# Optimization experiments

Measured on AMD Instinct MI355X. Metric: run time of the kernel, lower is better.

Reference implementation:

```python
import jax, jax.numpy as jnp
import numpy as np

D = 1024      # d_model
H = 16        # n_heads
KVH = 4       # num_kv_heads
DH = D // H   # head_dim = 64
CHUNK = 256
SDIM = 128
MG = 8        # m_global
B, T = 4, 4096


def setup_inputs() -> dict:
    key = jax.random.key(0)
    ks = jax.random.split(key, 12)
    s = 0.02
    mk = lambda i, shape: jax.random.normal(ks[i], shape, jnp.float32) * s
    return dict(
        x=jax.random.normal(ks[0], (B, T, D), jnp.float32),
        state=jnp.zeros((B, SDIM), jnp.float32),
        Wq=mk(1, (D, D)), Wk=mk(2, (KVH * DH, D)), Wv=mk(3, (KVH * DH, D)),
        Wo=mk(4, (D, D)), bo=jnp.zeros((D,), jnp.float32),
        ln_attn_g=jnp.ones((D,), jnp.float32), ln_attn_b=jnp.zeros((D,), jnp.float32),
        ln_ffn_g=jnp.ones((D,), jnp.float32), ln_ffn_b=jnp.zeros((D,), jnp.float32),
        W1=mk(5, (4 * D, D)), b1=jnp.zeros((4 * D,), jnp.float32),
        W2=mk(6, (D, 4 * D)), b2=jnp.zeros((D,), jnp.float32),
        Wsp=mk(7, (SDIM, D)), bsp=jnp.zeros((SDIM,), jnp.float32),
        Wsi=mk(8, (D, SDIM)), bsi=jnp.zeros((D,), jnp.float32),
        gtok=mk(9, (MG, D)),
    )


def _ln(x, g, b):
    m = x.mean(-1, keepdims=True)
    v = ((x - m) ** 2).mean(-1, keepdims=True)
    return (x - m) / jnp.sqrt(v + 1e-5) * g + b


def reference(x, state, Wq, Wk, Wv, Wo, bo, ln_attn_g, ln_attn_b,
              ln_ffn_g, ln_ffn_b, W1, b1, W2, b2, Wsp, bsp, Wsi, bsi, gtok):
    Bn, Tn, Dn = x.shape
    nchunks = Tn // CHUNK
    Tc = MG + CHUNK            # tokens per attention call (globals + chunk)
    G = H // KVH               # query heads per KV head
    causal = jnp.tril(jnp.ones((Tc, Tc), bool))
    scale = 1.0 / np.sqrt(DH).astype(np.float32)

    def step(st, chunk):  # st:[B,SDIM], chunk:[B,CHUNK,D]
        h = _ln(chunk, ln_attn_g, ln_attn_b) + (st @ Wsi.T + bsi)[:, None, :]
        h_in = jnp.concatenate([jnp.broadcast_to(gtok, (Bn, MG, Dn)), h], axis=1)
        q = (h_in @ Wq.T).reshape(Bn, Tc, H, DH)
        k = (h_in @ Wk.T).reshape(Bn, Tc, KVH, DH)
        v = (h_in @ Wv.T).reshape(Bn, Tc, KVH, DH)
        # GQA: group query heads over shared KV heads
        qg = q.reshape(Bn, Tc, KVH, G, DH)
        scores = jnp.einsum('bqhgd,bkhd->bhgqk', qg * scale, k)
        scores = jnp.where(causal, scores, -jnp.inf)
        attn = jax.nn.softmax(scores, axis=-1)
        o = jnp.einsum('bhgqk,bkhd->bqhgd', attn, v).reshape(Bn, Tc, Dn)
        y = (o @ Wo.T + bo)[:, MG:, :]
        c = chunk + y
        ff = jax.nn.gelu(_ln(c, ln_ffn_g, ln_ffn_b) @ W1.T + b1, approximate=False) @ W2.T + b2
        c = c + ff
        new_st = c.mean(axis=1) @ Wsp.T + bsp
        return new_st, c

    chunks = x.reshape(Bn, nchunks, CHUNK, Dn).transpose(1, 0, 2, 3)
    final_state, outs = jax.lax.scan(step, state, chunks)
    y_full = outs.transpose(1, 0, 2, 3).reshape(Bn, Tn, Dn)
    return y_full, final_state
```

## Files before the change

### kernel.cpp

```cpp
#include <hip/hip_runtime.h>
#include <hip/hip_bf16.h>

#define Dm    1024
#define Hn    16
#define KVH   4
#define DH    64
#define CHUNK 256
#define SDIM  128
#define MG    8
#define Bn    4
#define Tn    4096
#define TC    264
#define NSTEP 16
#define TD    4194304L

typedef __attribute__((ext_vector_type(8))) short short8;
typedef __attribute__((ext_vector_type(4))) float floatx4;
typedef __hip_bfloat16 bf16;

__device__ __forceinline__ void gl16(const void* g, void* l) {
    using GP = const __attribute__((address_space(1))) char*;
    using LP = __attribute__((address_space(3))) char*;
    __builtin_amdgcn_global_load_lds((GP)g, (LP)l, 16, 0, 0);
}


__global__ __launch_bounds__(512) void vcopy_k(const float* __restrict__ s, float* __restrict__ d, int n) {
    int i = blockIdx.x * 512 + threadIdx.x;
    if (i < n) d[i] = s[i];
}

__global__ __launch_bounds__(256) void cvt_bf16_k(const float* __restrict__ s, bf16* __restrict__ d, int n4) {
    int i = blockIdx.x * 256 + threadIdx.x;
    if (i >= n4) return;
    float4 v = ((const float4*)s)[i];
    bf16* o = d + i * 4;
    o[0] = __float2bfloat16(v.x); o[1] = __float2bfloat16(v.y);
    o[2] = __float2bfloat16(v.z); o[3] = __float2bfloat16(v.w);
}

__global__ __launch_bounds__(256) void fill_globals_k(const float* __restrict__ gtok, bf16* __restrict__ h_in) {
    int idx = blockIdx.x * 256 + threadIdx.x;
    int b = idx >> 13, rd = idx & 8191;
    h_in[(long)b * (TC * Dm) + rd] = __float2bfloat16(gtok[rd]);
}

__global__ __launch_bounds__(64) void state_proj_k(const float* __restrict__ st, const float* __restrict__ Wsi,
                                                   const float* __restrict__ bsi, float* __restrict__ si) {
    int b = blockIdx.x, g = blockIdx.y;
    int d = g * 64 + threadIdx.x;
    const float* sr = st + b * SDIM;
    const float* wr = Wsi + (long)d * SDIM;
    float a = bsi[d];
#pragma unroll
    for (int k4 = 0; k4 < 32; ++k4) {
        float4 sv = *(const float4*)(sr + k4 * 4);
        float4 wv = *(const float4*)(wr + k4 * 4);
        a += sv.x * wv.x + sv.y * wv.y + sv.z * wv.z + sv.w * wv.w;
    }
    si[b * Dm + d] = a;
}

__global__ __launch_bounds__(256) void ln_rows_k(const float* __restrict__ in, long inS, long inRoff,
                                                 bf16* __restrict__ out, long outS, long outRoff,
                                                 const float* __restrict__ g, const float* __restrict__ be,
                                                 const float* __restrict__ add) {
    int r = blockIdx.x, b = blockIdx.y, tid = threadIdx.x;
    const float* row = in + (long)b * inS + (inRoff + r) * (long)Dm;
    float4 v = *(const float4*)(row + tid * 4);
    float s = v.x + v.y + v.z + v.w;
    float q = v.x * v.x + v.y * v.y + v.z * v.z + v.w * v.w;
    for (int off = 32; off > 0; off >>= 1) { s += __shfl_down(s, off); q += __shfl_down(q, off); }
    __shared__ float red[10];
    int w = tid >> 6;
    if ((tid & 63) == 0) { red[w] = s; red[4 + w] = q; }
    __syncthreads();
    if (tid == 0) {
        float ts = red[0] + red[1] + red[2] + red[3];
        float tq = red[4] + red[5] + red[6] + red[7];
        float mean = ts * (1.f / Dm);
        float var = tq * (1.f / Dm) - mean * mean;
        red[8] = mean;
        red[9] = rsqrtf(var + 1e-5f);
    }
    __syncthreads();
    float mean = red[8], rstd = red[9];
    int d = tid * 4;
    float4 gv = *(const float4*)(g + d);
    float4 bv = *(const float4*)(be + d);
    float o0 = (v.x - mean) * rstd * gv.x + bv.x;
    float o1 = (v.y - mean) * rstd * gv.y + bv.y;
    float o2 = (v.z - mean) * rstd * gv.z + bv.z;
    float o3 = (v.w - mean) * rstd * gv.w + bv.w;
    if (add) {
        float4 av = *(const float4*)(add + b * Dm + d);
        o0 += av.x; o1 += av.y; o2 += av.z; o3 += av.w;
    }
    bf16* orow = out + (long)b * outS + (outRoff + r) * (long)Dm + d;
    orow[0] = __float2bfloat16(o0); orow[1] = __float2bfloat16(o1);
    orow[2] = __float2bfloat16(o2); orow[3] = __float2bfloat16(o3);
}

template<int BN>
__global__ __launch_bounds__(256) void gemm64(
    const bf16* __restrict__ A, const bf16* __restrict__ W,
    int M, int N, int K, int kspan,
    bf16* __restrict__ Cb, int ldc, const float* __restrict__ bias, int gelu,
    float* __restrict__ Cpart, long partMN)
{
    constexpr int NSEG = 4 + BN / 16;
    constexpr int SEGW = NSEG / 4;
    constexpr int FC   = BN / 64;
    constexpr int WN   = BN / 4;
    __shared__ short S[2 * NSEG * 512];

    int tid = threadIdx.x;
    int w = tid >> 6, l = tid & 63;
    int m0 = blockIdx.y << 6, n0 = blockIdx.x * BN;
    int kb = blockIdx.z * kspan;

    const bf16* gp[SEGW];
    int so[SEGW];
#pragma unroll
    for (int si = 0; si < SEGW; ++si) {
        int s = w + si * 4;
        const bf16* base = (s < 4) ? (A + (long)(m0 + s * 16 + (l >> 2)) * K)
                                   : (W + (long)(n0 + (s - 4) * 16 + (l >> 2)) * K);
        gp[si] = base + ((l & 3) << 3) + kb;
        so[si] = s * 1024 + l * 16;
    }
    char* cS = (char*)S;
    constexpr int LDSB = NSEG * 1024;

    floatx4 acc[4][FC];
#pragma unroll
    for (int t = 0; t < 4; ++t)
#pragma unroll
        for (int u = 0; u < FC; ++u) acc[t][u] = (floatx4){0.f, 0.f, 0.f, 0.f};

    int arow = l & 15;
    int acol = (l >> 4) << 3;
    int nk = kspan >> 5;

#define STAGE(t)                                                     \
    {                                                                \
        int kt_ = (t) << 5;                                          \
        char* b_ = cS + (((t) & 1) ? LDSB : 0);                      \
        _Pragma("unroll")                                            \
        for (int si = 0; si < SEGW; ++si) gl16(gp[si] + kt_, b_ + so[si]); \
    }

    STAGE(0)
    for (int i = 0; i < nk; ++i) {
        if (i + 1 < nk) {
            STAGE(i + 1)
            if constexpr (SEGW == 2) asm volatile("s_waitcnt vmcnt(2)" ::: "memory");
            else                     asm volatile("s_waitcnt vmcnt(3)" ::: "memory");
        } else {
            asm volatile("s_waitcnt vmcnt(0)" ::: "memory");
        }
        __builtin_amdgcn_s_barrier();
        __builtin_amdgcn_sched_barrier(0);
        const short* buf = S + (i & 1) * (NSEG * 512);
        short8 a[4], b[FC];
#pragma unroll
        for (int t = 0; t < 4; ++t)
            a[t] = *(const short8*)&buf[(t * 16 + arow) * 32 + acol];
#pragma unroll
        for (int u = 0; u < FC; ++u)
            b[u] = *(const short8*)&buf[2048 + (w * WN + u * 16 + arow) * 32 + acol];
#pragma unroll
        for (int t = 0; t < 4; ++t)
#pragma unroll
            for (int u = 0; u < FC; ++u)
                acc[t][u] = __builtin_amdgcn_mfma_f32_16x16x32_bf16(a[t], b[u], acc[t][u], 0, 0, 0);
        __builtin_amdgcn_sched_barrier(0);
        __builtin_amdgcn_s_barrier();
    }
#undef STAGE

    int crow0 = m0 + ((l >> 4) << 2);
    int ccol0 = n0 + w * WN + (l & 15);
    if (Cpart) {
        float* pp = Cpart + (long)blockIdx.z * partMN;
#pragma unroll
        for (int t = 0; t < 4; ++t)
#pragma unroll
            for (int rr = 0; rr < 4; ++rr) {
                int m = crow0 + t * 16 + rr;
                if (m >= M) continue;
#pragma unroll
                for (int u = 0; u < FC; ++u)
                    pp[(long)m * N + ccol0 + u * 16] = acc[t][u][rr];
            }
    } else {
#pragma unroll
        for (int t = 0; t < 4; ++t)
#pragma unroll
            for (int rr = 0; rr < 4; ++rr) {
                int m = crow0 + t * 16 + rr;
                if (m >= M) continue;
                bf16* crow = Cb + (long)m * ldc;
#pragma unroll
                for (int u = 0; u < FC; ++u) {
                    int n = ccol0 + u * 16;
                    float v = acc[t][u][rr];
                    if (bias) v += bias[n];
                    if (gelu) v = 0.5f * v * (1.f + erff(v * 0.70710678118654752f));
                    crow[n] = __float2bfloat16(v);
                }
            }
    }
}

__global__ __launch_bounds__(256) void reduce_splitk_k(const float* __restrict__ part, int KS,
                                                       const float* __restrict__ bias,
                                                       const float* __restrict__ res,
                                                       float* __restrict__ out, long roff) {
    int e4 = blockIdx.x * 256 + threadIdx.x;
    int m = e4 >> 8, n4 = e4 & 255;
    float4 s = ((const float4*)part)[e4];
    for (int z = 1; z < KS; ++z) {
        float4 p = ((const float4*)(part + (long)z * 1048576))[e4];
        s.x += p.x; s.y += p.y; s.z += p.z; s.w += p.w;
    }
    float4 bv = ((const float4*)bias)[n4];
    long ro = (long)(m >> 8) * TD + (roff + (m & 255)) * 1024L + n4 * 4;
    float4 rv = *(const float4*)(res + ro);
    s.x += bv.x + rv.x; s.y += bv.y + rv.y; s.z += bv.z + rv.z; s.w += bv.w + rv.w;
    *(float4*)(out + ro) = s;
}

__global__ __launch_bounds__(256) void reduce_ln_k(const float* __restrict__ part,
                                                   const float* __restrict__ bo,
                                                   const float* __restrict__ x,
                                                   float* __restrict__ out, long roff,
                                                   const float* __restrict__ g,
                                                   const float* __restrict__ be,
                                                   bf16* __restrict__ t_ln) {
    int m = blockIdx.x;
    int b = m >> 8, r = m & 255;
    int tid = threadIdx.x;
    long ro = (long)b * TD + (roff + r) * 1024L + tid * 4;
    int pi = m * 256 + tid;
    float4 s  = ((const float4*)part)[pi];
    float4 p2 = ((const float4*)(part + 1048576))[pi];
    float4 bv = ((const float4*)bo)[tid];
    float4 rv = *(const float4*)(x + ro);
    float c0 = s.x + p2.x + bv.x + rv.x;
    float c1 = s.y + p2.y + bv.y + rv.y;
    float c2 = s.z + p2.z + bv.z + rv.z;
    float c3 = s.w + p2.w + bv.w + rv.w;
    *(float4*)(out + ro) = make_float4(c0, c1, c2, c3);
    float sum = c0 + c1 + c2 + c3;
    float sq  = c0 * c0 + c1 * c1 + c2 * c2 + c3 * c3;
    for (int off = 32; off > 0; off >>= 1) { sum += __shfl_down(sum, off); sq += __shfl_down(sq, off); }
    __shared__ float red[10];
    int w = tid >> 6;
    if ((tid & 63) == 0) { red[w] = sum; red[4 + w] = sq; }
    __syncthreads();
    if (tid == 0) {
        float ts = red[0] + red[1] + red[2] + red[3];
        float tq = red[4] + red[5] + red[6] + red[7];
        float mean = ts * (1.f / Dm);
        float var = tq * (1.f / Dm) - mean * mean;
        red[8] = mean;
        red[9] = rsqrtf(var + 1e-5f);
    }
    __syncthreads();
    float mean = red[8], rstd = red[9];
    float4 gv = ((const float4*)g)[tid];
    float4 bev = ((const float4*)be)[tid];
    bf16* orow = t_ln + (long)(b * CHUNK + r) * Dm + tid * 4;
    orow[0] = __float2bfloat16((c0 - mean) * rstd * gv.x + bev.x);
    orow[1] = __float2bfloat16((c1 - mean) * rstd * gv.y + bev.y);
    orow[2] = __float2bfloat16((c2 - mean) * rstd * gv.z + bev.z);
    orow[3] = __float2bfloat16((c3 - mean) * rstd * gv.w + bev.w);
}

__global__ __launch_bounds__(256) void attn_mfma_k(const bf16* __restrict__ qkv, bf16* __restrict__ o_mat) {
    int qc = blockIdx.x, head = blockIdx.y, b = blockIdx.z;
    int kvh = head >> 2;
    int tid = threadIdx.x, w = tid >> 6, l = tid & 63;
    int m16 = l & 15, h4 = l >> 4;

    __shared__ short Qs[64][64];
    __shared__ short Ks[64][64];
    __shared__ short Vt[64][64];
    __shared__ short Ps[4][16][64];

    const long rowq0 = (long)b * TC + MG + qc * 64;
    const bf16* kbase = qkv + ((long)b * TC) * 1536 + 1024 + kvh * DH;
    const bf16* vbase = kbase + 256;

#pragma unroll
    for (int p = 0; p < 2; ++p) {
        int rr = p * 32 + (tid >> 3);
        gl16(qkv + (rowq0 + rr) * 1536 + head * DH + (tid & 7) * 8, &Qs[rr][(tid & 7) * 8]);
    }

    float a_m[4] = {-1e30f, -1e30f, -1e30f, -1e30f};
    float a_l[4] = {0.f, 0.f, 0.f, 0.f};
    floatx4 acc_o[4];
#pragma unroll
    for (int dt = 0; dt < 4; ++dt) acc_o[dt] = (floatx4){0.f, 0.f, 0.f, 0.f};
    short8 aq[2];

    int qtok0 = MG + qc * 64 + w * 16 + h4 * 4;
    int ntiles = qc + 2;

    for (int t = 0; t < ntiles; ++t) {
        int jt = t * 64;
#pragma unroll
        for (int p = 0; p < 2; ++p) {
            int rr = p * 32 + (tid >> 3);
            int gk = min(jt + rr, TC - 1);
            gl16(kbase + (long)gk * 1536 + (tid & 7) * 8, &Ks[rr][(tid & 7) * 8]);
        }
#pragma unroll
        for (int p = 0; p < 2; ++p) {
            int cg = p * 4 + w;
            int gk = min(jt + l, TC - 1);
            short8 vv = *(const short8*)(vbase + (long)gk * 1536 + cg * 8);
#pragma unroll
            for (int e = 0; e < 8; ++e) Vt[cg * 8 + e][l] = vv[e];
        }
        __syncthreads();
        if (t == 0) {
            aq[0] = *(const short8*)&Qs[w * 16 + m16][h4 * 8];
            aq[1] = *(const short8*)&Qs[w * 16 + m16][32 + h4 * 8];
        }
        floatx4 s[4];
#pragma unroll
        for (int st = 0; st < 4; ++st) {
            s[st] = (floatx4){0.f, 0.f, 0.f, 0.f};
#pragma unroll
            for (int c = 0; c < 2; ++c) {
                short8 kf = *(const short8*)&Ks[st * 16 + m16][c * 32 + h4 * 8];
                s[st] = __builtin_amdgcn_mfma_f32_16x16x32_bf16(aq[c], kf, s[st], 0, 0, 0);
            }
        }
#pragma unroll
        for (int st = 0; st < 4; ++st) {
            int keyg = jt + st * 16 + m16;
#pragma unroll
            for (int r = 0; r < 4; ++r) {
                float v = s[st][r] * 0.125f;
                s[st][r] = (keyg > qtok0 + r) ? -1e30f : v;
            }
        }
#pragma unroll
        for (int r = 0; r < 4; ++r) {
            float tm = fmaxf(fmaxf(s[0][r], s[1][r]), fmaxf(s[2][r], s[3][r]));
            tm = fmaxf(tm, __shfl_xor(tm, 1));
            tm = fmaxf(tm, __shfl_xor(tm, 2));
            tm = fmaxf(tm, __shfl_xor(tm, 4));
            tm = fmaxf(tm, __shfl_xor(tm, 8));
            float mn = fmaxf(a_m[r], tm);
            float rs = __expf(a_m[r] - mn);
            a_m[r] = mn;
            float ps = 0.f;
#pragma unroll
            for (int st = 0; st < 4; ++st) {
                float p = __expf(s[st][r] - mn);
                s[st][r] = p;
                ps += p;
            }
            ps += __shfl_xor(ps, 1); ps += __shfl_xor(ps, 2);
            ps += __shfl_xor(ps, 4); ps += __shfl_xor(ps, 8);
            a_l[r] = a_l[r] * rs + ps;
#pragma unroll
            for (int dt = 0; dt < 4; ++dt) acc_o[dt][r] *= rs;
#pragma unroll
            for (int st = 0; st < 4; ++st) {
                bf16 hb = __float2bfloat16(s[st][r]);
                Ps[w][h4 * 4 + r][st * 16 + m16] = *reinterpret_cast<short*>(&hb);
            }
        }
#pragma unroll
        for (int c = 0; c < 2; ++c) {
            short8 ap = *(const short8*)&Ps[w][m16][c * 32 + h4 * 8];
#pragma unroll
            for (int dt = 0; dt < 4; ++dt) {
                short8 vf = *(const short8*)&Vt[dt * 16 + m16][c * 32 + h4 * 8];
                acc_o[dt] = __builtin_amdgcn_mfma_f32_16x16x32_bf16(ap, vf, acc_o[dt], 0, 0, 0);
            }
        }
        __syncthreads();
    }

#pragma unroll
    for (int r = 0; r < 4; ++r) {
        float inv = 1.f / a_l[r];
        long row = (long)b * CHUNK + qc * 64 + w * 16 + h4 * 4 + r;
#pragma unroll
        for (int dt = 0; dt < 4; ++dt)
            o_mat[row * Dm + head * DH + dt * 16 + m16] = __float2bfloat16(acc_o[dt][r] * inv);
    }
}

__global__ __launch_bounds__(256) void col_part_k(const float* __restrict__ c, long stepOff,
                                                  float* __restrict__ colp) {
    int b = blockIdx.x, rg = blockIdx.y;
    int d4 = threadIdx.x;
    const float* base = c + (long)b * TD + stepOff + (long)(rg * 32) * Dm + d4 * 4;
    float4 s = make_float4(0.f, 0.f, 0.f, 0.f);
    for (int r = 0; r < 32; ++r) {
        float4 v = *(const float4*)(base + (long)r * Dm);
        s.x += v.x; s.y += v.y; s.z += v.z; s.w += v.w;
    }
    *(float4*)(colp + ((b * 8 + rg) << 10) + d4 * 4) = s;
}

__global__ __launch_bounds__(256) void state_update_k(const float* __restrict__ colp,
                                                      const float* __restrict__ Wsp,
                                                      const float* __restrict__ bsp,
                                                      float* __restrict__ st) {
    int b = blockIdx.x;
    int tid = threadIdx.x, w = tid >> 6, l = tid & 63;
    int ss = blockIdx.y * 4 + w;
    float4 m[4];
#pragma unroll
    for (int t = 0; t < 4; ++t) m[t] = make_float4(0.f, 0.f, 0.f, 0.f);
    for (int rg = 0; rg < 8; ++rg) {
        const float* pr = colp + ((b * 8 + rg) << 10) + l * 16;
#pragma unroll
        for (int t = 0; t < 4; ++t) {
            float4 v = *(const float4*)(pr + t * 4);
            m[t].x += v.x; m[t].y += v.y; m[t].z += v.z; m[t].w += v.w;
        }
    }
    const float* wr = Wsp + (long)ss * Dm + l * 16;
    float a = 0.f;
#pragma unroll
    for (int t = 0; t < 4; ++t) {
        float4 wv = *(const float4*)(wr + t * 4);
        a += m[t].x * wv.x + m[t].y * wv.y + m[t].z * wv.z + m[t].w * wv.w;
    }
    a *= (1.f / CHUNK);
    for (int off = 32; off > 0; off >>= 1) a += __shfl_down(a, off);
    if (l == 0) st[b * SDIM + ss] = a + bsp[ss];
}


extern "C" void kernel_launch(void* const* d_in, const int* in_sizes, int n_in,
                              void* d_out, int out_size, void* d_ws, size_t ws_size,
                              hipStream_t stream) {
    const float* x     = (const float*)d_in[0];
    const float* state = (const float*)d_in[1];
    const float* Wq    = (const float*)d_in[2];
    const float* Wk    = (const float*)d_in[3];
    const float* Wv    = (const float*)d_in[4];
    const float* Wo    = (const float*)d_in[5];
    const float* bo    = (const float*)d_in[6];
    const float* lag   = (const float*)d_in[7];
    const float* lab   = (const float*)d_in[8];
    const float* lfg   = (const float*)d_in[9];
    const float* lfb   = (const float*)d_in[10];
    const float* W1    = (const float*)d_in[11];
    const float* b1    = (const float*)d_in[12];
    const float* W2    = (const float*)d_in[13];
    const float* b2    = (const float*)d_in[14];
    const float* Wsp   = (const float*)d_in[15];
    const float* bsp   = (const float*)d_in[16];
    const float* Wsi   = (const float*)d_in[17];
    const float* bsi   = (const float*)d_in[18];
    const float* gtok  = (const float*)d_in[19];

    float* out = (float*)d_out;
    char*  wsb = (char*)d_ws;

    bf16* wqkv  = (bf16*)(wsb);
    bf16* wo    = (bf16*)(wsb + 3145728);
    bf16* w1    = (bf16*)(wsb + 5242880);
    bf16* w2    = (bf16*)(wsb + 13631488);
    bf16* h_in  = (bf16*)(wsb + 22020096);
    char* scrA  = wsb + 24379392;
    bf16* qkvb  = (bf16*)scrA;
    bf16* u     = (bf16*)scrA;
    char* scrB  = wsb + 32768000;
    bf16* o_mat = (bf16*)scrB;
    bf16* t_ln  = (bf16*)scrB;
    float* colp = (float*)scrB;
    float* si     = (float*)(wsb + 34865152);
    float* st     = (float*)(wsb + 34897920);
    float* part   = (float*)(wsb + 34901248);

    vcopy_k<<<1, 512, 0, stream>>>(state, st, 512);
    cvt_bf16_k<<<1024, 256, 0, stream>>>(Wq, wqkv,            262144);
    cvt_bf16_k<<< 256, 256, 0, stream>>>(Wk, wqkv + 1048576,   65536);
    cvt_bf16_k<<< 256, 256, 0, stream>>>(Wv, wqkv + 1310720,   65536);
    cvt_bf16_k<<<1024, 256, 0, stream>>>(Wo, wo,              262144);
    cvt_bf16_k<<<4096, 256, 0, stream>>>(W1, w1,             1048576);
    cvt_bf16_k<<<4096, 256, 0, stream>>>(W2, w2,             1048576);
    fill_globals_k<<<128, 256, 0, stream>>>(gtok, h_in);

    for (int s = 0; s < NSTEP; ++s) {
        long roff = (long)s * CHUNK;
        state_proj_k<<<dim3(4, 16), 64, 0, stream>>>(st, Wsi, bsi, si);
        ln_rows_k<<<dim3(256, 4), 256, 0, stream>>>(x, TD, roff, h_in, (long)TC * Dm, MG, lag, lab, si);
        gemm64<64><<<dim3(24, 17, 1), 256, 0, stream>>>(
            h_in, wqkv, Bn * TC, 1536, 1024, 1024,
            qkvb, 1536, nullptr, 0, nullptr, 0L);
        attn_mfma_k<<<dim3(4, 16, 4), 256, 0, stream>>>(qkvb, o_mat);
        gemm64<64><<<dim3(16, 16, 2), 256, 0, stream>>>(
            o_mat, wo, Bn * CHUNK, 1024, 1024, 512,
            nullptr, 0, nullptr, 0, part, 1048576L);
        reduce_ln_k<<<1024, 256, 0, stream>>>(part, bo, x, out, roff, lfg, lfb, t_ln);
        gemm64<128><<<dim3(32, 16, 1), 256, 0, stream>>>(
            t_ln, w1, Bn * CHUNK, 4096, 1024, 1024,
            u, 4096, b1, 1, nullptr, 0L);
        gemm64<64><<<dim3(16, 16, 2), 256, 0, stream>>>(
            u, w2, Bn * CHUNK, 1024, 4096, 2048,
            nullptr, 0, nullptr, 0, part, 1048576L);
        reduce_splitk_k<<<1024, 256, 0, stream>>>(part, 2, b2, out, out, roff);
        col_part_k<<<dim3(4, 8), 256, 0, stream>>>(out, roff * Dm, colp);
        state_update_k<<<dim3(4, 32), 256, 0, stream>>>(colp, Wsp, bsp, st);
    }
    vcopy_k<<<1, 512, 0, stream>>>(st, out + (long)Bn * Tn * Dm, 512);
}
```

Baseline: 1.711 ms.

## Hoist state term out of QKV GEMM and batch four chunks per projection

The state-injection term goes through Wqkv algebraically: a fused Wqkv·Wsi matrix and bias are precomputed once, so the QKV projection of LayerNorm'd x no longer depends on the recurrent state. That projection is batched across four chunks into one larger GEMM, and each step only adds a small per-batch state bias to its chunk's q/k/v. The split-K reduce and column-sum kernels are fused, and the GEMM now stages 64-wide K per barrier. It adds bf16 rounding of the fused weights and q/k/v before the state add, which may shift numerics.

Measured after the change: 1.580 ms. -7.6%, faster.

```diff
diff --git a/kernel.cpp b/kernel.cpp
--- a/kernel.cpp
+++ b/kernel.cpp
@@ -23,6 +23,14 @@
     using LP = __attribute__((address_space(3))) char*;
     __builtin_amdgcn_global_load_lds((GP)g, (LP)l, 16, 0, 0);
 }
+__device__ __forceinline__ float b2f(short s) {
+    unsigned int u = ((unsigned int)(unsigned short)s) << 16;
+    float f; __builtin_memcpy(&f, &u, 4); return f;
+}
+__device__ __forceinline__ short f2b(float f) {
+    bf16 h = __float2bfloat16(f);
+    short s; __builtin_memcpy(&s, &h, 2); return s;
+}
 
 
 __global__ __launch_bounds__(512) void vcopy_k(const float* __restrict__ s, float* __restrict__ d, int n) {
@@ -39,34 +47,64 @@
     o[2] = __float2bfloat16(v.z); o[3] = __float2bfloat16(v.w);
 }
 
-__global__ __launch_bounds__(256) void fill_globals_k(const float* __restrict__ gtok, bf16* __restrict__ h_in) {
+__global__ __launch_bounds__(256) void wsiT_k(const float* __restrict__ Wsi, bf16* __restrict__ WsiT) {
     int idx = blockIdx.x * 256 + threadIdx.x;
-    int b = idx >> 13, rd = idx & 8191;
-    h_in[(long)b * (TC * Dm) + rd] = __float2bfloat16(gtok[rd]);
-}
-
-__global__ __launch_bounds__(64) void state_proj_k(const float* __restrict__ st, const float* __restrict__ Wsi,
-                                                   const float* __restrict__ bsi, float* __restrict__ si) {
-    int b = blockIdx.x, g = blockIdx.y;
-    int d = g * 64 + threadIdx.x;
+    int s = idx >> 10, d = idx & 1023;
+    WsiT[idx] = __float2bfloat16(Wsi[d * SDIM + s]);
+}
+
+__global__ __launch_bounds__(64) void bfused_k(const bf16* __restrict__ wqkv, const float* __restrict__ bsi,
+                                               float* __restrict__ bfused) {
+    int n = blockIdx.x * 64 + threadIdx.x;
+    const bf16* wr = wqkv + (long)n * 1024;
+    float a = 0.f;
+    for (int k8 = 0; k8 < 128; ++k8) {
+        short8 wv = *(const short8*)(wr + k8 * 8);
+#pragma unroll
+        for (int e = 0; e < 8; ++e) a += b2f(wv[e]) * bsi[k8 * 8 + e];
+    }
+    bfused[n] = a;
+}
+
+__global__ __launch_bounds__(64) void sib_k(const float* __restrict__ st, const bf16* __restrict__ Wf,
+                                            const float* __restrict__ bfused, float* __restrict__ sib) {
+    int b = blockIdx.x, n = blockIdx.y * 64 + threadIdx.x;
     const float* sr = st + b * SDIM;
-    const float* wr = Wsi + (long)d * SDIM;
-    float a = bsi[d];
-#pragma unroll
-    for (int k4 = 0; k4 < 32; ++k4) {
-        float4 sv = *(const float4*)(sr + k4 * 4);
-        float4 wv = *(const float4*)(wr + k4 * 4);
-        a += sv.x * wv.x + sv.y * wv.y + sv.z * wv.z + sv.w * wv.w;
-    }
-    si[b * Dm + d] = a;
-}
-
-__global__ __launch_bounds__(256) void ln_rows_k(const float* __restrict__ in, long inS, long inRoff,
-                                                 bf16* __restrict__ out, long outS, long outRoff,
-                                                 const float* __restrict__ g, const float* __restrict__ be,
-                                                 const float* __restrict__ add) {
-    int r = blockIdx.x, b = blockIdx.y, tid = threadIdx.x;
-    const float* row = in + (long)b * inS + (inRoff + r) * (long)Dm;
+    const bf16* wr = Wf + (long)n * SDIM;
+    float a = bfused[n];
+#pragma unroll
+    for (int k8 = 0; k8 < 16; ++k8) {
+        short8 wv = *(const short8*)(wr + k8 * 8);
+#pragma unroll
+        for (int e = 0; e < 8; ++e) a += sr[k8 * 8 + e] * b2f(wv[e]);
+    }
+    sib[b * 1536 + n] = a;
+}
+
+__global__ __launch_bounds__(192) void addsi_k(bf16* __restrict__ qkv_s, const float* __restrict__ sib) {
+    int b = blockIdx.x, r = MG + blockIdx.y, n0 = threadIdx.x * 8;
+    bf16* p = qkv_s + ((long)(b * TC + r) * 1536 + n0);
+    const float* sb = sib + b * 1536 + n0;
+    short8 v = *(const short8*)p;
+    short8 o;
+#pragma unroll
+    for (int e = 0; e < 8; ++e) o[e] = f2b(b2f(v[e]) + sb[e]);
+    *(short8*)p = o;
+}
+
+__global__ __launch_bounds__(256) void lng_k(const float* __restrict__ x, const float* __restrict__ gtok,
+                                             const float* __restrict__ g, const float* __restrict__ be,
+                                             bf16* __restrict__ lnxg, int gstep) {
+    int bx = blockIdx.x, b = blockIdx.y, tid = threadIdx.x;
+    int sl = bx / 264, r = bx - sl * 264;
+    bf16* orow = lnxg + (long)((sl * 4 + b) * 264 + r) * 1024 + tid * 4;
+    if (r < MG) {
+        float4 v = *(const float4*)(gtok + r * 1024 + tid * 4);
+        orow[0] = __float2bfloat16(v.x); orow[1] = __float2bfloat16(v.y);
+        orow[2] = __float2bfloat16(v.z); orow[3] = __float2bfloat16(v.w);
+        return;
+    }
+    const float* row = x + (long)b * TD + ((long)(gstep * 4 + sl) * 256 + (r - MG)) * 1024;
     float4 v = *(const float4*)(row + tid * 4);
     float s = v.x + v.y + v.z + v.w;
     float q = v.x * v.x + v.y * v.y + v.z * v.z + v.w * v.w;
@@ -88,17 +126,10 @@
     int d = tid * 4;
     float4 gv = *(const float4*)(g + d);
     float4 bv = *(const float4*)(be + d);
-    float o0 = (v.x - mean) * rstd * gv.x + bv.x;
-    float o1 = (v.y - mean) * rstd * gv.y + bv.y;
-    float o2 = (v.z - mean) * rstd * gv.z + bv.z;
-    float o3 = (v.w - mean) * rstd * gv.w + bv.w;
-    if (add) {
-        float4 av = *(const float4*)(add + b * Dm + d);
-        o0 += av.x; o1 += av.y; o2 += av.z; o3 += av.w;
-    }
-    bf16* orow = out + (long)b * outS + (outRoff + r) * (long)Dm + d;
-    orow[0] = __float2bfloat16(o0); orow[1] = __float2bfloat16(o1);
-    orow[2] = __float2bfloat16(o2); orow[3] = __float2bfloat16(o3);
+    orow[0] = __float2bfloat16((v.x - mean) * rstd * gv.x + bv.x);
+    orow[1] = __float2bfloat16((v.y - mean) * rstd * gv.y + bv.y);
+    orow[2] = __float2bfloat16((v.z - mean) * rstd * gv.z + bv.z);
+    orow[3] = __float2bfloat16((v.w - mean) * rstd * gv.w + bv.w);
 }
 
 template<int BN>
@@ -112,12 +143,14 @@
     constexpr int SEGW = NSEG / 4;
     constexpr int FC   = BN / 64;
     constexpr int WN   = BN / 4;
-    __shared__ short S[2 * NSEG * 512];
+    constexpr int HALFB = NSEG * 1024;
+    constexpr int PHB   = 2 * HALFB;
+    __shared__ short S[PHB];
 
     int tid = threadIdx.x;
     int w = tid >> 6, l = tid & 63;
     int m0 = blockIdx.y << 6, n0 = blockIdx.x * BN;
-    int kb = blockIdx.z * kspan;
+    long kb = (long)blockIdx.z * kspan;
 
     const bf16* gp[SEGW];
     int so[SEGW];
@@ -130,7 +163,6 @@
         so[si] = s * 1024 + l * 16;
     }
     char* cS = (char*)S;
-    constexpr int LDSB = NSEG * 1024;
 
     floatx4 acc[4][FC];
 #pragma unroll
@@ -140,40 +172,47 @@
 
     int arow = l & 15;
     int acol = (l >> 4) << 3;
-    int nk = kspan >> 5;
-
-#define STAGE(t)                                                     \
-    {                                                                \
-        int kt_ = (t) << 5;                                          \
-        char* b_ = cS + (((t) & 1) ? LDSB : 0);                      \
-        _Pragma("unroll")                                            \
-        for (int si = 0; si < SEGW; ++si) gl16(gp[si] + kt_, b_ + so[si]); \
+    int np = kspan >> 6;
+
+#define STAGE(p)                                                         \
+    {                                                                    \
+        int kt_ = (p) << 6;                                              \
+        char* b_ = cS + ((p) & 1) * PHB;                                 \
+        _Pragma("unroll")                                                \
+        for (int si = 0; si < SEGW; ++si) {                              \
+            gl16(gp[si] + kt_, b_ + so[si]);                             \
+            gl16(gp[si] + kt_ + 32, b_ + HALFB + so[si]);                \
+        }                                                                \
     }
 
     STAGE(0)
-    for (int i = 0; i < nk; ++i) {
-        if (i + 1 < nk) {
-            STAGE(i + 1)
-            if constexpr (SEGW == 2) asm volatile("s_waitcnt vmcnt(2)" ::: "memory");
-            else                     asm volatile("s_waitcnt vmcnt(3)" ::: "memory");
+    for (int p = 0; p < np; ++p) {
+        if (p + 1 < np) {
+            STAGE(p + 1)
+            if constexpr (SEGW == 2) asm volatile("s_waitcnt vmcnt(4)" ::: "memory");
+            else                     asm volatile("s_waitcnt vmcnt(6)" ::: "memory");
         } else {
             asm volatile("s_waitcnt vmcnt(0)" ::: "memory");
         }
         __builtin_amdgcn_s_barrier();
         __builtin_amdgcn_sched_barrier(0);
-        const short* buf = S + (i & 1) * (NSEG * 512);
-        short8 a[4], b[FC];
-#pragma unroll
-        for (int t = 0; t < 4; ++t)
-            a[t] = *(const short8*)&buf[(t * 16 + arow) * 32 + acol];
-#pragma unroll
-        for (int u = 0; u < FC; ++u)
-            b[u] = *(const short8*)&buf[2048 + (w * WN + u * 16 + arow) * 32 + acol];
-#pragma unroll
-        for (int t = 0; t < 4; ++t)
+        const short* buf = S + (p & 1) * (PHB / 2);
+#pragma unroll
+        for (int kh = 0; kh < 2; ++kh) {
+            const short* hb = buf + kh * (HALFB / 2);
+            short8 a[4], b[FC];
+#pragma unroll
+            for (int t = 0; t < 4; ++t)
+                a[t] = *(const short8*)&hb[(t * 16 + arow) * 32 + acol];
 #pragma unroll
             for (int u = 0; u < FC; ++u)
-                acc[t][u] = __builtin_amdgcn_mfma_f32_16x16x32_bf16(a[t], b[u], acc[t][u], 0, 0, 0);
+                b[u] = *(const short8*)&hb[2048 + (w * WN + u * 16 + arow) * 32 + acol];
+#pragma unroll
+            for (int t = 0; t < 4; ++t)
+#pragma unroll
+                for (int u = 0; u < FC; ++u)
+                    acc[t][u] = __builtin_amdgcn_mfma_f32_16x16x32_bf16(a[t], b[u], acc[t][u], 0, 0, 0);
+        }
         __builtin_amdgcn_sched_barrier(0);
         __builtin_amdgcn_s_barrier();
     }
@@ -211,24 +250,6 @@
                 }
             }
     }
-}
-
-__global__ __launch_bounds__(256) void reduce_splitk_k(const float* __restrict__ part, int KS,
-                                                       const float* __restrict__ bias,
-                                                       const float* __restrict__ res,
-                                                       float* __restrict__ out, long roff) {
-    int e4 = blockIdx.x * 256 + threadIdx.x;
-    int m = e4 >> 8, n4 = e4 & 255;
-    float4 s = ((const float4*)part)[e4];
-    for (int z = 1; z < KS; ++z) {
-        float4 p = ((const float4*)(part + (long)z * 1048576))[e4];
-        s.x += p.x; s.y += p.y; s.z += p.z; s.w += p.w;
-    }
-    float4 bv = ((const float4*)bias)[n4];
-    long ro = (long)(m >> 8) * TD + (roff + (m & 255)) * 1024L + n4 * 4;
-    float4 rv = *(const float4*)(res + ro);
-    s.x += bv.x + rv.x; s.y += bv.y + rv.y; s.z += bv.z + rv.z; s.w += bv.w + rv.w;
-    *(float4*)(out + ro) = s;
 }
 
 __global__ __launch_bounds__(256) void reduce_ln_k(const float* __restrict__ part,
@@ -278,6 +299,29 @@
     orow[3] = __float2bfloat16((c3 - mean) * rstd * gv.w + bev.w);
 }
 
+__global__ __launch_bounds__(256) void reduce_colpart_k(const float* __restrict__ part,
+                                                        const float* __restrict__ bias,
+                                                        float* __restrict__ out, long roff,
+                                                        float* __restrict__ colp) {
+    int b = blockIdx.x, rg = blockIdx.y, tid = threadIdx.x;
+    float4 bv = ((const float4*)bias)[tid];
+    float4 cs = make_float4(0.f, 0.f, 0.f, 0.f);
+#pragma unroll
+    for (int r8 = 0; r8 < 8; ++r8) {
+        int r = rg * 8 + r8;
+        int pi = (b * 256 + r) * 256 + tid;
+        float4 s  = ((const float4*)part)[pi];
+        float4 p2 = ((const float4*)(part + 1048576))[pi];
+        long ro = (long)b * TD + (roff + r) * 1024L + tid * 4;
+        float4 rv = *(const float4*)(out + ro);
+        float4 v = make_float4(s.x + p2.x + bv.x + rv.x, s.y + p2.y + bv.y + rv.y,
+                               s.z + p2.z + bv.z + rv.z, s.w + p2.w + bv.w + rv.w);
+        *(float4*)(out + ro) = v;
+        cs.x += v.x; cs.y += v.y; cs.z += v.z; cs.w += v.w;
+    }
+    *(float4*)(colp + ((b * 32 + rg) << 10) + tid * 4) = cs;
+}
+
 __global__ __launch_bounds__(256) void attn_mfma_k(const bf16* __restrict__ qkv, bf16* __restrict__ o_mat) {
     int qc = blockIdx.x, head = blockIdx.y, b = blockIdx.z;
     int kvh = head >> 2;
@@ -373,8 +417,7 @@
             for (int dt = 0; dt < 4; ++dt) acc_o[dt][r] *= rs;
 #pragma unroll
             for (int st = 0; st < 4; ++st) {
-                bf16 hb = __float2bfloat16(s[st][r]);
-                Ps[w][h4 * 4 + r][st * 16 + m16] = *reinterpret_cast<short*>(&hb);
+                Ps[w][h4 * 4 + r][st * 16 + m16] = f2b(s[st][r]);
             }
         }
 #pragma unroll
@@ -397,19 +440,6 @@
         for (int dt = 0; dt < 4; ++dt)
             o_mat[row * Dm + head * DH + dt * 16 + m16] = __float2bfloat16(acc_o[dt][r] * inv);
     }
-}
-
-__global__ __launch_bounds__(256) void col_part_k(const float* __restrict__ c, long stepOff,
-                                                  float* __restrict__ colp) {
-    int b = blockIdx.x, rg = blockIdx.y;
-    int d4 = threadIdx.x;
-    const float* base = c + (long)b * TD + stepOff + (long)(rg * 32) * Dm + d4 * 4;
-    float4 s = make_float4(0.f, 0.f, 0.f, 0.f);
-    for (int r = 0; r < 32; ++r) {
-        float4 v = *(const float4*)(base + (long)r * Dm);
-        s.x += v.x; s.y += v.y; s.z += v.z; s.w += v.w;
-    }
-    *(float4*)(colp + ((b * 8 + rg) << 10) + d4 * 4) = s;
 }
 
 __global__ __launch_bounds__(256) void state_update_k(const float* __restrict__ colp,
@@ -422,8 +452,8 @@
     float4 m[4];
 #pragma unroll
     for (int t = 0; t < 4; ++t) m[t] = make_float4(0.f, 0.f, 0.f, 0.f);
-    for (int rg = 0; rg < 8; ++rg) {
-        const float* pr = colp + ((b * 8 + rg) << 10) + l * 16;
+    for (int rg = 0; rg < 32; ++rg) {
+        const float* pr = colp + ((b * 32 + rg) << 10) + l * 16;
 #pragma unroll
         for (int t = 0; t < 4; ++t) {
             float4 v = *(const float4*)(pr + t * 4);
@@ -470,21 +500,24 @@
     float* out = (float*)d_out;
     char*  wsb = (char*)d_ws;
 
-    bf16* wqkv  = (bf16*)(wsb);
-    bf16* wo    = (bf16*)(wsb + 3145728);
-    bf16* w1    = (bf16*)(wsb + 5242880);
-    bf16* w2    = (bf16*)(wsb + 13631488);
-    bf16* h_in  = (bf16*)(wsb + 22020096);
-    char* scrA  = wsb + 24379392;
-    bf16* qkvb  = (bf16*)scrA;
-    bf16* u     = (bf16*)scrA;
-    char* scrB  = wsb + 32768000;
-    bf16* o_mat = (bf16*)scrB;
-    bf16* t_ln  = (bf16*)scrB;
-    float* colp = (float*)scrB;
-    float* si     = (float*)(wsb + 34865152);
-    float* st     = (float*)(wsb + 34897920);
-    float* part   = (float*)(wsb + 34901248);
+    bf16* wqkv   = (bf16*)(wsb);
+    bf16* wo     = (bf16*)(wsb + 3145728);
+    bf16* w1     = (bf16*)(wsb + 5242880);
+    bf16* w2     = (bf16*)(wsb + 13631488);
+    bf16* Wfused = (bf16*)(wsb + 22020096);
+    bf16* WsiT   = (bf16*)(wsb + 22413312);
+    float* bfused= (float*)(wsb + 22675456);
+    float* sib   = (float*)(wsb + 22681600);
+    float* st    = (float*)(wsb + 22706176);
+    bf16* qkvg   = (bf16*)(wsb + 22708224);
+    char* R1     = wsb + 35684352;
+    bf16* lnxg   = (bf16*)R1;
+    bf16* u      = (bf16*)R1;
+    float* part  = (float*)(wsb + 44335104);
+    char* scrB   = wsb + 52723712;
+    bf16* o_mat  = (bf16*)scrB;
+    bf16* t_ln   = (bf16*)scrB;
+    float* colp  = (float*)scrB;
 
     vcopy_k<<<1, 512, 0, stream>>>(state, st, 512);
     cvt_bf16_k<<<1024, 256, 0, stream>>>(Wq, wqkv,            262144);
@@ -493,16 +526,25 @@
     cvt_bf16_k<<<1024, 256, 0, stream>>>(Wo, wo,              262144);
     cvt_bf16_k<<<4096, 256, 0, stream>>>(W1, w1,             1048576);
     cvt_bf16_k<<<4096, 256, 0, stream>>>(W2, w2,             1048576);
-    fill_globals_k<<<128, 256, 0, stream>>>(gtok, h_in);
+    wsiT_k<<<512, 256, 0, stream>>>(Wsi, WsiT);
+    gemm64<64><<<dim3(2, 24, 1), 256, 0, stream>>>(
+        wqkv, WsiT, 1536, 128, 1024, 1024,
+        Wfused, 128, nullptr, 0, nullptr, 0L);
+    bfused_k<<<24, 64, 0, stream>>>(wqkv, bsi, bfused);
 
     for (int s = 0; s < NSTEP; ++s) {
         long roff = (long)s * CHUNK;
-        state_proj_k<<<dim3(4, 16), 64, 0, stream>>>(st, Wsi, bsi, si);
-        ln_rows_k<<<dim3(256, 4), 256, 0, stream>>>(x, TD, roff, h_in, (long)TC * Dm, MG, lag, lab, si);
-        gemm64<64><<<dim3(24, 17, 1), 256, 0, stream>>>(
-            h_in, wqkv, Bn * TC, 1536, 1024, 1024,
-            qkvb, 1536, nullptr, 0, nullptr, 0L);
-        attn_mfma_k<<<dim3(4, 16, 4), 256, 0, stream>>>(qkvb, o_mat);
+        if ((s & 3) == 0) {
+            int g = s >> 2;
+            lng_k<<<dim3(1056, 4), 256, 0, stream>>>(x, gtok, lag, lab, lnxg, g);
+            gemm64<64><<<dim3(24, 66, 1), 256, 0, stream>>>(
+                lnxg, wqkv, 4224, 1536, 1024, 1024,
+                qkvg, 1536, nullptr, 0, nullptr, 0L);
+        }
+        bf16* qkv_s = qkvg + (long)(s & 3) * (4 * 264 * 1536);
+        sib_k<<<dim3(4, 24), 64, 0, stream>>>(st, Wfused, bfused, sib);
+        addsi_k<<<dim3(4, 256), 192, 0, stream>>>(qkv_s, sib);
+        attn_mfma_k<<<dim3(4, 16, 4), 256, 0, stream>>>(qkv_s, o_mat);
         gemm64<64><<<dim3(16, 16, 2), 256, 0, stream>>>(
             o_mat, wo, Bn * CHUNK, 1024, 1024, 512,
             nullptr, 0, nullptr, 0, part, 1048576L);
@@ -513,8 +555,7 @@
         gemm64<64><<<dim3(16, 16, 2), 256, 0, stream>>>(
             u, w2, Bn * CHUNK, 1024, 4096, 2048,
             nullptr, 0, nullptr, 0, part, 1048576L);
-        reduce_splitk_k<<<1024, 256, 0, stream>>>(part, 2, b2, out, out, roff);
-        col_part_k<<<dim3(4, 8), 256, 0, stream>>>(out, roff * Dm, colp);
+        reduce_colpart_k<<<dim3(4, 32), 256, 0, stream>>>(part, b2, out, roff, colp);
         state_update_k<<<dim3(4, 32), 256, 0, stream>>>(colp, Wsp, bsp, st);
     }
     vcopy_k<<<1, 512, 0, stream>>>(st, out + (long)Bn * Tn * Dm, 512);
```
